# Optimization experiments

Hardware: AMD Instinct MI355X
Metric: run time of the kernel (lower is better)

Reference implementation:

```python
import jax, jax.numpy as jnp
import numpy as np

NEG_NUM = -10000.0
PRUNE_L, PRUNE_R = -3, 3  # prune_range


def setup_inputs() -> dict:
    key = jax.random.key(0)
    ks = jax.random.split(key, 8)
    B, L, D_CTX, D_Q, H = 32, 2048, 512, 1024, 256
    s = 0.02
    query = jax.random.normal(ks[0], (B, D_Q), jnp.float32)
    ctx = jax.random.normal(ks[1], (B, L, D_CTX), jnp.float32)
    # previous kappa (attention centre) spread over the source positions
    kappa_prev = jax.random.uniform(ks[2], (B, 1), jnp.float32) * L
    Wq = jax.random.normal(ks[3], (D_Q, H), jnp.float32) * s
    bq = jnp.zeros((H,), jnp.float32)
    Ws = jax.random.normal(ks[4], (H, 3), jnp.float32) * s
    # bias init: alpha_bias=0, beta_bias=-1, kappa_bias=-1
    bs = jnp.array([0.0, -1.0, -1.0], jnp.float32)
    W1 = jax.random.normal(ks[5], (D_CTX + D_Q, H), jnp.float32) * s
    b1 = jnp.zeros((H,), jnp.float32)
    W2 = jax.random.normal(ks[6], (H, 1), jnp.float32) * s
    b2 = jnp.zeros((1,), jnp.float32)
    return dict(query=query, ctx=ctx, kappa_prev=kappa_prev, Wq=Wq, bq=bq,
                Ws=Ws, bs=bs, W1=W1, b1=b1, W2=W2, b2=b2)


def reference(query, ctx, kappa_prev, Wq, bq, Ws, bs, W1, b1, W2, b2):
    B, L, D_CTX = ctx.shape
    # stat projection: alpha/beta/kappa (n_mixtures = 1)
    h = jnp.tanh(query @ Wq + bq)                       # [B, H]
    stat = h @ Ws + bs                                  # [B, 3]
    alpha = jnp.exp(stat[:, 0:1])                       # [B, 1]
    beta = jnp.exp(stat[:, 1:2])                        # [B, 1]
    kappa = jnp.exp(stat[:, 2:3]) + kappa_prev          # monotonic: [B, 1]

    pos = jnp.arange(L, dtype=jnp.float32)              # [L]
    diff = pos[None, :] - kappa                         # [B, L]
    prior = alpha * jnp.exp(-beta * diff * diff)        # [B, L]

    # local prune window around round(kappa) (mask built on detached kappa)
    center = jnp.round(jax.lax.stop_gradient(kappa))    # [B, 1]
    mask = (pos[None, :] >= center + PRUNE_L) & (pos[None, :] <= center + PRUNE_R)
    prior = jnp.where(mask, prior, 0.0)                 # [B, L]

    # MLP likelihood scorer over (ctx, query)
    q_exp = jnp.broadcast_to(query[:, None, :], (B, L, query.shape[1]))
    comb = jnp.concatenate([ctx, q_exp], axis=-1)       # [B, L, D_CTX+D_Q]
    score = (jnp.tanh(comb @ W1 + b1) @ W2 + b2)[..., 0]  # [B, L]
    score = jnp.where(mask, score, NEG_NUM)
    likelihood = jnp.exp(score)                         # [B, L]

    posterior = jnp.where(mask, likelihood * prior, 0.0)  # [B, L]
    p_ctx = posterior / jnp.sum(posterior, axis=-1, keepdims=True)  # normalize_post
    expected_ctx = jnp.einsum('bl,bld->bd', p_ctx, ctx)  # [B, D_CTX]
    return expected_ctx, p_ctx
```

## Files before the change

kernel.cpp:

```cpp
#include <hip/hip_runtime.h>
#include <cmath>

constexpr int B     = 32;
constexpr int L     = 2048;
constexpr int D_CTX = 512;
constexpr int D_Q   = 1024;
constexpr int H     = 256;
constexpr int PRUNE_L = -3;
constexpr int PRUNE_R = 3;
constexpr int W = PRUNE_R - PRUNE_L + 1;
constexpr int KC = 16;

__global__ __launch_bounds__(256) void partial_kernel(
    const float* __restrict__ query,
    const float* __restrict__ Wq,
    const float* __restrict__ W1,
    float* __restrict__ partQ,
    float* __restrict__ part1)
{
    const int kc = blockIdx.x;
    const int b  = blockIdx.y;
    const int j  = threadIdx.x;
    const int k0 = kc * (D_Q / KC);

    __shared__ float q_sh[D_Q / KC];
    if (j < D_Q / KC) q_sh[j] = query[b * D_Q + k0 + j];
    __syncthreads();

    const float* WqR = Wq + (size_t)k0 * H + j;
    const float* W1R = W1 + ((size_t)D_CTX + k0) * H + j;
    float accQ = 0.f, acc1 = 0.f;
#pragma unroll 16
    for (int k = 0; k < D_Q / KC; ++k) {
        const float qk = q_sh[k];
        accQ += qk * WqR[(size_t)k * H];
        acc1 += qk * W1R[(size_t)k * H];
    }
    partQ[((size_t)b * KC + kc) * H + j] = accQ;
    part1[((size_t)b * KC + kc) * H + j] = acc1;
}

__global__ __launch_bounds__(256) void stats_kernel(
    const float* __restrict__ kappa_prev,
    const float* __restrict__ bq,
    const float* __restrict__ Ws,
    const float* __restrict__ bs,
    const float* __restrict__ b1,
    const float* __restrict__ partQ,
    const float* __restrict__ part1,
    float* __restrict__ stats,
    float* __restrict__ qpre)
{
    const int b = blockIdx.x;
    const int j = threadIdx.x;

    float sq = 0.f, s1 = 0.f;
#pragma unroll
    for (int kc = 0; kc < KC; ++kc) {
        sq += partQ[((size_t)b * KC + kc) * H + j];
        s1 += part1[((size_t)b * KC + kc) * H + j];
    }
    __shared__ float h_sh[H];
    h_sh[j] = tanhf(sq + bq[j]);
    qpre[(size_t)b * H + j] = s1 + b1[j];
    __syncthreads();

    if (j < 64) {
        float s0 = 0.f, s1r = 0.f, s2 = 0.f;
#pragma unroll
        for (int i = 0; i < 4; ++i) {
            const int   jj = j + 64 * i;
            const float hv = h_sh[jj];
            s0  += hv * Ws[jj * 3 + 0];
            s1r += hv * Ws[jj * 3 + 1];
            s2  += hv * Ws[jj * 3 + 2];
        }
        for (int off = 32; off > 0; off >>= 1) {
            s0  += __shfl_down(s0, off);
            s1r += __shfl_down(s1r, off);
            s2  += __shfl_down(s2, off);
        }
        if (j == 0) {
            const float alpha = expf(s0 + bs[0]);
            const float beta  = expf(s1r + bs[1]);
            const float kappa = expf(s2 + bs[2]) + kappa_prev[b];
            stats[b * 4 + 0] = alpha;
            stats[b * 4 + 1] = beta;
            stats[b * 4 + 2] = kappa;
            stats[b * 4 + 3] = rintf(kappa);
        }
    }
}

__global__ __launch_bounds__(512) void score_kernel(
    const float* __restrict__ ctx,
    const float* __restrict__ W1,
    const float* __restrict__ W2,
    const float* __restrict__ b2,
    const float* __restrict__ stats,
    const float* __restrict__ qpre,
    float* __restrict__ post)
{
    const int t   = blockIdx.x;
    const int b   = blockIdx.y;
    const int tid = threadIdx.x;
    const int jg  = tid & 63;
    const int kc  = tid >> 6;

    const float alpha  = stats[b * 4 + 0];
    const float beta   = stats[b * 4 + 1];
    const float kappa  = stats[b * 4 + 2];
    const int   center = (int)stats[b * 4 + 3];
    const int   l      = center + PRUNE_L + t;

    if (l < 0 || l >= L) {
        if (tid == 0) post[b * W + t] = 0.0f;
        return;
    }

    __shared__ float  c_sh[D_CTX];
    __shared__ float4 part[8][64];
    __shared__ float  red[H];

    const float4* ctx4 = (const float4*)(ctx + ((size_t)b * L + (size_t)l) * D_CTX);
    if (tid < D_CTX / 4) ((float4*)c_sh)[tid] = ctx4[tid];
    __syncthreads();

    const float4* Wv = (const float4*)W1;
    float4 acc = make_float4(0.f, 0.f, 0.f, 0.f);
    const int k0 = kc * 64;
#pragma unroll 8
    for (int k = k0; k < k0 + 64; ++k) {
        const float  ck = c_sh[k];
        const float4 w  = Wv[k * 64 + jg];
        acc.x += ck * w.x; acc.y += ck * w.y;
        acc.z += ck * w.z; acc.w += ck * w.w;
    }
    part[kc][jg] = acc;
    __syncthreads();
    for (int s = 4; s > 0; s >>= 1) {
        if (kc < s) {
            float4 a = part[kc][jg], c = part[kc + s][jg];
            a.x += c.x; a.y += c.y; a.z += c.z; a.w += c.w;
            part[kc][jg] = a;
        }
        __syncthreads();
    }
    if (tid < H) {
        const float pre = ((const float*)part)[tid] + qpre[(size_t)b * H + tid];
        red[tid] = tanhf(pre) * W2[tid];
    }
    __syncthreads();
    for (int s = H / 2; s > 0; s >>= 1) {
        if (tid < s) red[tid] += red[tid + s];
        __syncthreads();
    }
    if (tid == 0) {
        const float score = red[0] + b2[0];
        const float diff  = (float)l - kappa;
        post[b * W + t] = expf(score) * alpha * expf(-beta * diff * diff);
    }
}

__global__ __launch_bounds__(256) void combine_kernel(
    const float* __restrict__ ctx,
    const float* __restrict__ stats,
    const float* __restrict__ post,
    float* __restrict__ out_e,
    float* __restrict__ out_p)
{
    const int b = blockIdx.x;
    const int j = threadIdx.x;

    __shared__ float p_sh[W];
    __shared__ int   l_sh[W];
    if (j == 0) {
        const int center = (int)stats[b * 4 + 3];
        float sum = 0.0f;
        for (int t = 0; t < W; ++t) sum += post[b * W + t];
        const float inv = 1.0f / sum;
        for (int t = 0; t < W; ++t) {
            p_sh[t] = post[b * W + t] * inv;
            l_sh[t] = center + PRUNE_L + t;
        }
    }
    __syncthreads();

    float4* prow = (float4*)(out_p + (size_t)b * L);
    const float4 z = make_float4(0.f, 0.f, 0.f, 0.f);
    prow[j]       = z;
    prow[j + 256] = z;
    __syncthreads();
    if (j < W) {
        const int l = l_sh[j];
        if (l >= 0 && l < L) out_p[(size_t)b * L + l] = p_sh[j];
    }

    if (j < D_CTX / 4) {
        float4 acc = make_float4(0.f, 0.f, 0.f, 0.f);
#pragma unroll
        for (int t = 0; t < W; ++t) {
            const int l = l_sh[t];
            if (l >= 0 && l < L) {
                const float4 c = ((const float4*)(ctx + ((size_t)b * L + (size_t)l) * D_CTX))[j];
                const float  p = p_sh[t];
                acc.x += p * c.x; acc.y += p * c.y;
                acc.z += p * c.z; acc.w += p * c.w;
            }
        }
        ((float4*)(out_e + (size_t)b * D_CTX))[j] = acc;
    }
}

extern "C" void kernel_launch(void* const* d_in, const int* in_sizes, int n_in,
                              void* d_out, int out_size, void* d_ws, size_t ws_size,
                              hipStream_t stream) {
    const float* query      = (const float*)d_in[0];
    const float* ctx        = (const float*)d_in[1];
    const float* kappa_prev = (const float*)d_in[2];
    const float* Wq         = (const float*)d_in[3];
    const float* bq         = (const float*)d_in[4];
    const float* Ws         = (const float*)d_in[5];
    const float* bs         = (const float*)d_in[6];
    const float* W1         = (const float*)d_in[7];
    const float* b1         = (const float*)d_in[8];
    const float* W2         = (const float*)d_in[9];
    const float* b2         = (const float*)d_in[10];

    float* out   = (float*)d_out;
    float* out_e = out;
    float* out_p = out + B * D_CTX;

    float* stats = (float*)d_ws;
    float* qpre  = stats + B * 4;
    float* post  = qpre + B * H;
    float* partQ = post + B * W + 8;
    float* part1 = partQ + B * KC * H;

    partial_kernel<<<dim3(KC, B), 256, 0, stream>>>(query, Wq, W1, partQ, part1);
    stats_kernel<<<B, 256, 0, stream>>>(kappa_prev, bq, Ws, bs, b1,
                                        partQ, part1, stats, qpre);
    score_kernel<<<dim3(W, B), 512, 0, stream>>>(ctx, W1, W2, b2, stats, qpre, post);
    combine_kernel<<<B, 256, 0, stream>>>(ctx, stats, post, out_e, out_p);
}
```

Before: 201.9 us.

## Fuse stats, score and combine kernels using last-block atomic counter

Merges the stats, score and combine kernels into one launch. Each of the W blocks per batch recomputes the stat projection and query pre-activation redundantly in shared memory, and the last block to finish (found through an atomic counter reset in the partial kernel) does the normalization and the weighted context sum. This removes two kernel launches and the round trips through global memory for the intermediates, at the cost of redundant partial-sum reads and extra threadfence/atomic synchronization.

```diff
diff --git a/kernel.cpp b/kernel.cpp
--- a/kernel.cpp
+++ b/kernel.cpp
@@ -16,12 +16,15 @@
     const float* __restrict__ Wq,
     const float* __restrict__ W1,
     float* __restrict__ partQ,
-    float* __restrict__ part1)
+    float* __restrict__ part1,
+    unsigned int* __restrict__ cnt)
 {
     const int kc = blockIdx.x;
     const int b  = blockIdx.y;
     const int j  = threadIdx.x;
     const int k0 = kc * (D_Q / KC);
+
+    if (kc == 0 && j == 0) cnt[b] = 0u;
 
     __shared__ float q_sh[D_Q / KC];
     if (j < D_Q / KC) q_sh[j] = query[b * D_Q + k0 + j];
@@ -40,7 +43,11 @@
     part1[((size_t)b * KC + kc) * H + j] = acc1;
 }
 
-__global__ __launch_bounds__(256) void stats_kernel(
+__global__ __launch_bounds__(512) void fused_kernel(
+    const float* __restrict__ ctx,
+    const float* __restrict__ W1,
+    const float* __restrict__ W2,
+    const float* __restrict__ b2,
     const float* __restrict__ kappa_prev,
     const float* __restrict__ bq,
     const float* __restrict__ Ws,
@@ -48,167 +55,167 @@
     const float* __restrict__ b1,
     const float* __restrict__ partQ,
     const float* __restrict__ part1,
-    float* __restrict__ stats,
-    float* __restrict__ qpre)
-{
-    const int b = blockIdx.x;
-    const int j = threadIdx.x;
-
-    float sq = 0.f, s1 = 0.f;
-#pragma unroll
-    for (int kc = 0; kc < KC; ++kc) {
-        sq += partQ[((size_t)b * KC + kc) * H + j];
-        s1 += part1[((size_t)b * KC + kc) * H + j];
-    }
-    __shared__ float h_sh[H];
-    h_sh[j] = tanhf(sq + bq[j]);
-    qpre[(size_t)b * H + j] = s1 + b1[j];
-    __syncthreads();
-
-    if (j < 64) {
-        float s0 = 0.f, s1r = 0.f, s2 = 0.f;
-#pragma unroll
-        for (int i = 0; i < 4; ++i) {
-            const int   jj = j + 64 * i;
-            const float hv = h_sh[jj];
-            s0  += hv * Ws[jj * 3 + 0];
-            s1r += hv * Ws[jj * 3 + 1];
-            s2  += hv * Ws[jj * 3 + 2];
-        }
-        for (int off = 32; off > 0; off >>= 1) {
-            s0  += __shfl_down(s0, off);
-            s1r += __shfl_down(s1r, off);
-            s2  += __shfl_down(s2, off);
-        }
-        if (j == 0) {
-            const float alpha = expf(s0 + bs[0]);
-            const float beta  = expf(s1r + bs[1]);
-            const float kappa = expf(s2 + bs[2]) + kappa_prev[b];
-            stats[b * 4 + 0] = alpha;
-            stats[b * 4 + 1] = beta;
-            stats[b * 4 + 2] = kappa;
-            stats[b * 4 + 3] = rintf(kappa);
-        }
-    }
-}
-
-__global__ __launch_bounds__(512) void score_kernel(
-    const float* __restrict__ ctx,
-    const float* __restrict__ W1,
-    const float* __restrict__ W2,
-    const float* __restrict__ b2,
-    const float* __restrict__ stats,
-    const float* __restrict__ qpre,
-    float* __restrict__ post)
+    float* __restrict__ post,
+    unsigned int* __restrict__ cnt,
+    float* __restrict__ out_e,
+    float* __restrict__ out_p)
 {
     const int t   = blockIdx.x;
     const int b   = blockIdx.y;
     const int tid = threadIdx.x;
-    const int jg  = tid & 63;
-    const int kc  = tid >> 6;
-
-    const float alpha  = stats[b * 4 + 0];
-    const float beta   = stats[b * 4 + 1];
-    const float kappa  = stats[b * 4 + 2];
-    const int   center = (int)stats[b * 4 + 3];
-    const int   l      = center + PRUNE_L + t;
-
-    if (l < 0 || l >= L) {
-        if (tid == 0) post[b * W + t] = 0.0f;
-        return;
-    }
-
+
+    __shared__ float  h_sh[H];
+    __shared__ float  qpre_sh[H];
+    __shared__ float  sstat[4];
     __shared__ float  c_sh[D_CTX];
     __shared__ float4 part[8][64];
     __shared__ float  red[H];
 
-    const float4* ctx4 = (const float4*)(ctx + ((size_t)b * L + (size_t)l) * D_CTX);
-    if (tid < D_CTX / 4) ((float4*)c_sh)[tid] = ctx4[tid];
-    __syncthreads();
-
-    const float4* Wv = (const float4*)W1;
-    float4 acc = make_float4(0.f, 0.f, 0.f, 0.f);
-    const int k0 = kc * 64;
+    if (tid < H) {
+        float s = 0.f;
+#pragma unroll
+        for (int kc = 0; kc < KC; ++kc)
+            s += partQ[((size_t)b * KC + kc) * H + tid];
+        h_sh[tid] = tanhf(s + bq[tid]);
+    } else {
+        const int j = tid - H;
+        float s = 0.f;
+#pragma unroll
+        for (int kc = 0; kc < KC; ++kc)
+            s += part1[((size_t)b * KC + kc) * H + j];
+        qpre_sh[j] = s + b1[j];
+    }
+    __syncthreads();
+
+    if (tid < 64) {
+        float s0 = 0.f, s1 = 0.f, s2 = 0.f;
+#pragma unroll
+        for (int i = 0; i < 4; ++i) {
+            const int   jj = tid + 64 * i;
+            const float hv = h_sh[jj];
+            s0 += hv * Ws[jj * 3 + 0];
+            s1 += hv * Ws[jj * 3 + 1];
+            s2 += hv * Ws[jj * 3 + 2];
+        }
+        for (int off = 32; off > 0; off >>= 1) {
+            s0 += __shfl_down(s0, off);
+            s1 += __shfl_down(s1, off);
+            s2 += __shfl_down(s2, off);
+        }
+        if (tid == 0) {
+            const float alpha = expf(s0 + bs[0]);
+            const float beta  = expf(s1 + bs[1]);
+            const float kappa = expf(s2 + bs[2]) + kappa_prev[b];
+            sstat[0] = alpha;
+            sstat[1] = beta;
+            sstat[2] = kappa;
+            sstat[3] = rintf(kappa);
+        }
+    }
+    __syncthreads();
+
+    const float alpha  = sstat[0];
+    const float beta   = sstat[1];
+    const float kappa  = sstat[2];
+    const int   center = (int)sstat[3];
+    const int   l      = center + PRUNE_L + t;
+    const bool  valid  = (l >= 0 && l < L);
+
+    if (valid) {
+        const float4* ctx4 =
+            (const float4*)(ctx + ((size_t)b * L + (size_t)l) * D_CTX);
+        if (tid < D_CTX / 4) ((float4*)c_sh)[tid] = ctx4[tid];
+        __syncthreads();
+
+        const int jg = tid & 63;
+        const int kc = tid >> 6;
+        const float4* Wv = (const float4*)W1;
+        float4 acc = make_float4(0.f, 0.f, 0.f, 0.f);
+        const int k0 = kc * 64;
 #pragma unroll 8
-    for (int k = k0; k < k0 + 64; ++k) {
-        const float  ck = c_sh[k];
-        const float4 w  = Wv[k * 64 + jg];
-        acc.x += ck * w.x; acc.y += ck * w.y;
-        acc.z += ck * w.z; acc.w += ck * w.w;
-    }
-    part[kc][jg] = acc;
-    __syncthreads();
-    for (int s = 4; s > 0; s >>= 1) {
-        if (kc < s) {
-            float4 a = part[kc][jg], c = part[kc + s][jg];
-            a.x += c.x; a.y += c.y; a.z += c.z; a.w += c.w;
-            part[kc][jg] = a;
-        }
+        for (int k = k0; k < k0 + 64; ++k) {
+            const float  ck = c_sh[k];
+            const float4 w  = Wv[k * 64 + jg];
+            acc.x += ck * w.x; acc.y += ck * w.y;
+            acc.z += ck * w.z; acc.w += ck * w.w;
+        }
+        part[kc][jg] = acc;
         __syncthreads();
-    }
-    if (tid < H) {
-        const float pre = ((const float*)part)[tid] + qpre[(size_t)b * H + tid];
-        red[tid] = tanhf(pre) * W2[tid];
-    }
-    __syncthreads();
-    for (int s = H / 2; s > 0; s >>= 1) {
-        if (tid < s) red[tid] += red[tid + s];
+        for (int s = 4; s > 0; s >>= 1) {
+            if (kc < s) {
+                float4 a = part[kc][jg], c = part[kc + s][jg];
+                a.x += c.x; a.y += c.y; a.z += c.z; a.w += c.w;
+                part[kc][jg] = a;
+            }
+            __syncthreads();
+        }
+        if (tid < H) {
+            const float pre = ((const float*)part)[tid] + qpre_sh[tid];
+            red[tid] = tanhf(pre) * W2[tid];
+        }
         __syncthreads();
-    }
+        for (int s = H / 2; s > 0; s >>= 1) {
+            if (tid < s) red[tid] += red[tid + s];
+            __syncthreads();
+        }
+        if (tid == 0) {
+            const float score = red[0] + b2[0];
+            const float diff  = (float)l - kappa;
+            post[b * W + t] = expf(score) * alpha * expf(-beta * diff * diff);
+        }
+    } else {
+        if (tid == 0) post[b * W + t] = 0.0f;
+    }
+
+    __shared__ int last;
     if (tid == 0) {
-        const float score = red[0] + b2[0];
-        const float diff  = (float)l - kappa;
-        post[b * W + t] = expf(score) * alpha * expf(-beta * diff * diff);
-    }
-}
-
-__global__ __launch_bounds__(256) void combine_kernel(
-    const float* __restrict__ ctx,
-    const float* __restrict__ stats,
-    const float* __restrict__ post,
-    float* __restrict__ out_e,
-    float* __restrict__ out_p)
-{
-    const int b = blockIdx.x;
-    const int j = threadIdx.x;
+        __threadfence();
+        const unsigned int old = atomicAdd(&cnt[b], 1u);
+        last = (old == (unsigned int)(W - 1));
+    }
+    __syncthreads();
+    if (!last) return;
 
     __shared__ float p_sh[W];
     __shared__ int   l_sh[W];
-    if (j == 0) {
-        const int center = (int)stats[b * 4 + 3];
-        float sum = 0.0f;
-        for (int t = 0; t < W; ++t) sum += post[b * W + t];
+    if (tid == 0) {
+        __threadfence();
+        float pv[W];
+        float sum = 0.f;
+        for (int u = 0; u < W; ++u) {
+            pv[u] = ((volatile const float*)post)[b * W + u];
+            sum += pv[u];
+        }
         const float inv = 1.0f / sum;
-        for (int t = 0; t < W; ++t) {
-            p_sh[t] = post[b * W + t] * inv;
-            l_sh[t] = center + PRUNE_L + t;
+        for (int u = 0; u < W; ++u) {
+            p_sh[u] = pv[u] * inv;
+            l_sh[u] = center + PRUNE_L + u;
         }
     }
     __syncthreads();
 
     float4* prow = (float4*)(out_p + (size_t)b * L);
-    const float4 z = make_float4(0.f, 0.f, 0.f, 0.f);
-    prow[j]       = z;
-    prow[j + 256] = z;
-    __syncthreads();
-    if (j < W) {
-        const int l = l_sh[j];
-        if (l >= 0 && l < L) out_p[(size_t)b * L + l] = p_sh[j];
-    }
-
-    if (j < D_CTX / 4) {
+    prow[tid] = make_float4(0.f, 0.f, 0.f, 0.f);
+    __syncthreads();
+    if (tid < W) {
+        const int ll = l_sh[tid];
+        if (ll >= 0 && ll < L) out_p[(size_t)b * L + ll] = p_sh[tid];
+    }
+
+    if (tid < D_CTX / 4) {
         float4 acc = make_float4(0.f, 0.f, 0.f, 0.f);
 #pragma unroll
-        for (int t = 0; t < W; ++t) {
-            const int l = l_sh[t];
-            if (l >= 0 && l < L) {
-                const float4 c = ((const float4*)(ctx + ((size_t)b * L + (size_t)l) * D_CTX))[j];
-                const float  p = p_sh[t];
+        for (int u = 0; u < W; ++u) {
+            const int ll = l_sh[u];
+            if (ll >= 0 && ll < L) {
+                const float4 c =
+                    ((const float4*)(ctx + ((size_t)b * L + (size_t)ll) * D_CTX))[tid];
+                const float p = p_sh[u];
                 acc.x += p * c.x; acc.y += p * c.y;
                 acc.z += p * c.z; acc.w += p * c.w;
             }
         }
-        ((float4*)(out_e + (size_t)b * D_CTX))[j] = acc;
+        ((float4*)(out_e + (size_t)b * D_CTX))[tid] = acc;
     }
 }
 
@@ -231,15 +238,15 @@
     float* out_e = out;
     float* out_p = out + B * D_CTX;
 
-    float* stats = (float*)d_ws;
-    float* qpre  = stats + B * 4;
-    float* post  = qpre + B * H;
-    float* partQ = post + B * W + 8;
+    float* partQ = (float*)d_ws;
     float* part1 = partQ + B * KC * H;
-
-    partial_kernel<<<dim3(KC, B), 256, 0, stream>>>(query, Wq, W1, partQ, part1);
-    stats_kernel<<<B, 256, 0, stream>>>(kappa_prev, bq, Ws, bs, b1,
-                                        partQ, part1, stats, qpre);
-    score_kernel<<<dim3(W, B), 512, 0, stream>>>(ctx, W1, W2, b2, stats, qpre, post);
-    combine_kernel<<<B, 256, 0, stream>>>(ctx, stats, post, out_e, out_p);
+    float* post  = part1 + B * KC * H;
+    unsigned int* cnt = (unsigned int*)(post + B * W);
+
+    partial_kernel<<<dim3(KC, B), 256, 0, stream>>>(query, Wq, W1,
+                                                    partQ, part1, cnt);
+    fused_kernel<<<dim3(W, B), 512, 0, stream>>>(ctx, W1, W2, b2,
+                                                 kappa_prev, bq, Ws, bs, b1,
+                                                 partQ, part1, post, cnt,
+                                                 out_e, out_p);
 }
```

Result: no change. 203.1 us (+0.6%).
